# Kernel tuning notes

Hardware: AMD Instinct MI355X
Metric: run time of the kernel (lower is better)

## Reference

```python
import jax, jax.numpy as jnp
import numpy as np
import math
from jax.scipy.special import gammaln

D = 256
TOKEN_WEIGHT_TEMP = 0.5
BESSEL_TERMS = 50


def log_bessel_i(v, x, terms=BESSEL_TERMS):
    # log I_v(x) via truncated series, logsumexp-stabilized (same math as
    # torch max-subtract + exp-sum-log).
    x = jnp.clip(x, 1e-6)
    k = jnp.arange(terms, dtype=x.dtype)
    log_coef = (2.0 * k + v) * jnp.log(x[..., None] / 2.0) - (gammaln(k + 1.0) + gammaln(k + v + 1.0))
    return jax.nn.logsumexp(log_coef, axis=-1)


def vmf_A(kappa, d):
    kappa = jnp.clip(kappa, 1e-6)
    nu = 0.5 * d - 1.0
    A = jnp.exp(jnp.clip(log_bessel_i(nu + 1.0, kappa) - log_bessel_i(nu, kappa), -60.0, 0.0))
    return jnp.clip(A, 1e-8, 1.0 - 1e-6)


def vmf_logpartition(kappa, d):
    kappa = jnp.clip(kappa, 1e-6)
    nu = 0.5 * d - 1.0
    return nu * jnp.log(kappa) - 0.5 * d * math.log(2.0 * math.pi) - log_bessel_i(nu, kappa)


def vmf_entropy(kappa, d):
    kappa = jnp.clip(kappa, 1e-6)
    return -vmf_logpartition(kappa, d) - kappa * vmf_A(kappa, d)


def vmf_kl(kappa_p, mu_dot, kappa_q, d):
    kappa_p = jnp.clip(kappa_p, 1e-6)
    kappa_q = jnp.clip(kappa_q, 1e-6)
    logC_p = vmf_logpartition(kappa_p, d)
    logC_q = vmf_logpartition(kappa_q, d)
    A_p = vmf_A(kappa_p, d)
    return logC_p - logC_q + A_p * (kappa_p - kappa_q * mu_dot)


def setup_inputs() -> dict:
    key = jax.random.key(0)
    k1, k2, k3, k4 = jax.random.split(key, 4)
    B, Tq, N, Tt = 128, 32, 128, 32
    q = jax.random.normal(k1, (B, Tq, D), dtype=jnp.float32)
    q = q / jnp.linalg.norm(q, axis=-1, keepdims=True)
    t = jax.random.normal(k2, (N, Tt, D), dtype=jnp.float32)
    t = t / jnp.linalg.norm(t, axis=-1, keepdims=True)
    kq = jax.random.uniform(k3, (B, Tq), dtype=jnp.float32) * 50.0 + 1.0
    kt = jax.random.uniform(k4, (N, Tt), dtype=jnp.float32) * 50.0 + 1.0
    temp = jnp.asarray(0.07, dtype=jnp.float32)
    return {"query_tokens": q, "kappa_q_tokens": kq, "target_tokens": t, "kappa_t_tokens": kt, "temp": temp}


def reference(query_tokens, kappa_q_tokens, target_tokens, kappa_t_tokens, temp):
    bs = query_tokens.shape[0]
    labels = jnp.arange(bs)
    # sim: [B, N, T_t, T_q]
    sim_q2t = jnp.einsum('bqd,ntd->bntq', query_tokens, target_tokens)
    kappa_q_tokens = jnp.clip(kappa_q_tokens, 1e-6)
    kappa_t_tokens = jnp.clip(kappa_t_tokens, 1e-6)
    kq = kappa_q_tokens[:, None, None, :]   # [B,1,1,T_q]
    kt = kappa_t_tokens[None, :, :, None]   # [1,N,T_t,1]
    kl_q_t = vmf_kl(kq, sim_q2t, kt, D)
    kl_t_q = vmf_kl(kt, sim_q2t, kq, D)
    skl_qt = 0.5 * (kl_q_t + kl_t_q)
    score_q2t = -skl_qt                      # [B,N,T_t,T_q]
    max_score_i2t = score_q2t.max(axis=2)    # [B,N,T_q]
    entropy_q = vmf_entropy(kappa_q_tokens, D)  # [B,T_q]
    token_weights = jax.nn.softmax(-jax.lax.stop_gradient(entropy_q) / TOKEN_WEIGHT_TEMP, axis=-1)
    score_global = (max_score_i2t * token_weights[:, None, :]).sum(axis=-1)  # [B,N]
    logits_global = score_global / jnp.clip(temp, 1e-6)
    log_probs = jax.nn.log_softmax(logits_global, axis=-1)
    loss_each = -log_probs[jnp.arange(bs), labels]
    loss_itc = loss_each.mean()
    return (loss_itc, logits_global, score_global, entropy_q)
```

## Files before the change

kernel.cpp:

```cpp
#include <hip/hip_runtime.h>
#include <math.h>

typedef _Float16 half8  __attribute__((ext_vector_type(8)));
typedef _Float16 half4v __attribute__((ext_vector_type(4)));
typedef float    floatx4 __attribute__((ext_vector_type(4)));

#define DDIM 256

#define GLOAD_LDS16(g, l) \
    __builtin_amdgcn_global_load_lds((const __attribute__((address_space(1))) void*)(g), \
                                     (__attribute__((address_space(3))) void*)(l), 16, 0, 0)

__global__ void prep(const float* __restrict__ q, const float* __restrict__ t,
                     _Float16* __restrict__ Qh, _Float16* __restrict__ Th,
                     const float* __restrict__ kq, const float* __restrict__ kt,
                     float* __restrict__ Apq, float* __restrict__ kqc, float* __restrict__ uq,
                     float* __restrict__ wq,
                     float* __restrict__ At,  float* __restrict__ ktc, float* __restrict__ vt,
                     float* __restrict__ ent_out, float* __restrict__ loss) {
    int b = blockIdx.x;
    if (b < 2048) {
        const float* src = (b < 1024) ? q : t;
        _Float16*    dst = (b < 1024) ? Qh : Th;
        int i = ((b & 1023) * 1024) + threadIdx.x * 4;
        float4 v = *(const float4*)(src + i);
        half4v h;
        h[0] = (_Float16)v.x; h[1] = (_Float16)v.y; h[2] = (_Float16)v.z; h[3] = (_Float16)v.w;
        *(half4v*)(dst + i) = h;
        return;
    }

    __shared__ float slg_s[50];
    __shared__ float l128_s[50];
    int tid = threadIdx.x;

    if (b == 2048 && tid == 0) loss[0] = 0.f;

    if (tid < 64) {
        int lane = tid;
        float a = 0.f;
        if (lane >= 1 && lane < 50) a = logf((float)lane) + logf((float)(lane + 127));
        #pragma unroll
        for (int off = 1; off < 64; off <<= 1) {
            float tmp = __shfl_up(a, off, 64);
            if (lane >= off) a += tmp;
        }
        if (lane < 50) {
            slg_s[lane]  = 491.5534482233f + a;
            l128_s[lane] = logf((float)(lane + 128));
        }
    }
    __syncthreads();

    int tok  = (b - 2048) * 256 + tid;
    bool isQ = tok < 4096;
    float kap  = fmaxf(isQ ? kq[tok] : kt[tok - 4096], 1e-6f);
    float lkap = logf(kap);
    float lx   = lkap - 0.6931471805599453f;

    float m0 = -INFINITY, m1 = -INFINITY;
    #pragma unroll 10
    for (int k = 0; k < 50; ++k) {
        float c0 = fmaf((float)(2 * k + 127), lx, -slg_s[k]);
        float c1 = c0 + lx - l128_s[k];
        m0 = fmaxf(m0, c0);
        m1 = fmaxf(m1, c1);
    }
    float s0 = 0.f, s1 = 0.f;
    #pragma unroll 10
    for (int k = 0; k < 50; ++k) {
        float c0 = fmaf((float)(2 * k + 127), lx, -slg_s[k]);
        float c1 = c0 + lx - l128_s[k];
        s0 += expf(c0 - m0);
        s1 += expf(c1 - m1);
    }
    float logI0 = m0 + logf(s0);
    float logI1 = m1 + logf(s1);

    float A = expf(fminf(fmaxf(logI1 - logI0, -60.f), 0.f));
    A = fminf(fmaxf(A, 1e-8f), 1.f - 1e-6f);
    float logC = 127.f * lkap - 235.2482644983962f - logI0;
    float ent  = -logC - kap * A;

    if (isQ) {
        float x = -2.0f * ent;
        float m = x;
        #pragma unroll
        for (int off = 1; off < 32; off <<= 1) m = fmaxf(m, __shfl_xor(m, off, 64));
        float p = expf(x - m);
        float s = p;
        #pragma unroll
        for (int off = 1; off < 32; off <<= 1) s += __shfl_xor(s, off, 64);
        Apq[tok] = A; kqc[tok] = kap; uq[tok] = -0.5f * A * kap;
        wq[tok]  = p / s;
        ent_out[tok] = ent;
    } else {
        int tt = tok - 4096;
        At[tt] = A; ktc[tt] = kap; vt[tt] = -0.5f * A * kap;
    }
}

__global__ void __launch_bounds__(512, 2)
gemm_score(const _Float16* __restrict__ Qh, const _Float16* __restrict__ Th,
           const float* __restrict__ Apq, const float* __restrict__ kqc,
           const float* __restrict__ uq,  const float* __restrict__ wq,
           const float* __restrict__ At,  const float* __restrict__ ktc,
           const float* __restrict__ vt,  float* __restrict__ score_out) {
    __shared__ _Float16 Qs[2][256 * 64];
    __shared__ _Float16 Ts[2][256 * 64];
    int tid = threadIdx.x;
    int lane = tid & 63, wave = tid >> 6;
    int wr = wave >> 2, wc = wave & 3;
    int bx = blockIdx.x, by = blockIdx.y;

    floatx4 acc[8][4];
    #pragma unroll
    for (int i = 0; i < 8; ++i)
        #pragma unroll
        for (int j = 0; j < 4; ++j)
            acc[i][j] = (floatx4){0.f, 0.f, 0.f, 0.f};

    int l15 = lane & 15, lq = lane >> 4;
    int swz = l15 & 7;

    int rs = tid >> 3;
    int cl = tid & 7;
    int cg = cl ^ (rs & 7);
    const _Float16* gq = Qh + (size_t)(by * 256 + rs) * DDIM + cg * 8;
    const _Float16* gt = Th + (size_t)(bx * 256 + rs) * DDIM + cg * 8;
    int lbase = wave * 1024;

    #pragma unroll
    for (int it = 0; it < 4; ++it) {
        GLOAD_LDS16(gq + it * 64 * DDIM, (char*)Qs[0] + lbase + it * 8192);
        GLOAD_LDS16(gt + it * 64 * DDIM, (char*)Ts[0] + lbase + it * 8192);
    }

    #pragma unroll
    for (int kk = 0; kk < 4; ++kk) {
        int p = kk & 1;
        __syncthreads();
        if (kk < 3) {
            #pragma unroll
            for (int it = 0; it < 4; ++it) {
                GLOAD_LDS16(gq + it * 64 * DDIM + (kk + 1) * 64,
                            (char*)Qs[p ^ 1] + lbase + it * 8192);
                GLOAD_LDS16(gt + it * 64 * DDIM + (kk + 1) * 64,
                            (char*)Ts[p ^ 1] + lbase + it * 8192);
            }
        }
        #pragma unroll
        for (int ks = 0; ks < 2; ++ks) {
            half8 a[8], b[4];
            int chunk = (ks * 4 + lq) ^ swz;
            #pragma unroll
            for (int i = 0; i < 8; ++i)
                a[i] = *(const half8*)(Qs[p] + (wr * 128 + i * 16 + l15) * 64 + chunk * 8);
            #pragma unroll
            for (int j = 0; j < 4; ++j)
                b[j] = *(const half8*)(Ts[p] + (wc * 64 + j * 16 + l15) * 64 + chunk * 8);
            #pragma unroll
            for (int i = 0; i < 8; ++i)
                #pragma unroll
                for (int j = 0; j < 4; ++j)
                    acc[i][j] = __builtin_amdgcn_mfma_f32_16x16x32_f16(a[i], b[j], acc[i][j], 0, 0, 0);
        }
    }

    int colbase = bx * 256 + wc * 64 + l15;
    int rowbase = by * 256 + wr * 128 + lq * 4;
    #pragma unroll
    for (int bi = 0; bi < 4; ++bi) {
        #pragma unroll
        for (int bj = 0; bj < 2; ++bj) {
            float part = 0.f;
            #pragma unroll
            for (int ii = 0; ii < 2; ++ii) {
                int i  = bi * 2 + ii;
                int rg = rowbase + i * 16;
                float mx[4] = {-INFINITY, -INFINITY, -INFINITY, -INFINITY};
                #pragma unroll
                for (int jj = 0; jj < 2; ++jj) {
                    int j   = bj * 2 + jj;
                    int cg2 = colbase + j * 16;
                    float at_ = At[cg2], kt_ = ktc[cg2], v_ = vt[cg2];
                    floatx4 sim = acc[i][j];
                    #pragma unroll
                    for (int rr = 0; rr < 4; ++rr) {
                        float sc = uq[rg + rr] + v_ +
                                   0.5f * (Apq[rg + rr] * kt_ + at_ * kqc[rg + rr]) * sim[rr];
                        mx[rr] = fmaxf(mx[rr], sc);
                    }
                }
                #pragma unroll
                for (int msk = 1; msk <= 8; msk <<= 1)
                    #pragma unroll
                    for (int rr = 0; rr < 4; ++rr)
                        mx[rr] = fmaxf(mx[rr], __shfl_xor(mx[rr], msk, 64));
                if (l15 == 0) {
                    #pragma unroll
                    for (int rr = 0; rr < 4; ++rr)
                        part += wq[rg + rr] * mx[rr];
                }
            }
            part += __shfl_xor(part, 16, 64);
            part += __shfl_xor(part, 32, 64);
            if (lane == 0) {
                int b = by * 8 + wr * 4 + bi;
                int n = bx * 8 + wc * 2 + bj;
                score_out[b * 128 + n] = part;
            }
        }
    }
}

__global__ void softmax_loss(const float* __restrict__ score, const float* __restrict__ temp_p,
                             float* __restrict__ logits, float* __restrict__ loss) {
    int tid = threadIdx.x, lane = tid & 63, w = tid >> 6;
    int r = blockIdx.x * 8 + w;
    float temp = fmaxf(temp_p[0], 1e-6f);
    float inv = 1.0f / temp;

    float2 v = ((const float2*)(score + r * 128))[lane];
    v.x *= inv; v.y *= inv;
    float m = fmaxf(v.x, v.y);
    #pragma unroll
    for (int off = 1; off < 64; off <<= 1) m = fmaxf(m, __shfl_xor(m, off, 64));
    float e = expf(v.x - m) + expf(v.y - m);
    #pragma unroll
    for (int off = 1; off < 64; off <<= 1) e += __shfl_xor(e, off, 64);
    float lse = m + logf(e);

    ((float2*)(logits + r * 128))[lane] = v;

    if (lane == 0) {
        float le = lse - score[r * 129] * inv;
        atomicAdd(loss, le * (1.0f / 128.0f));
    }
}

extern "C" void kernel_launch(void* const* d_in, const int* in_sizes, int n_in,
                              void* d_out, int out_size, void* d_ws, size_t ws_size,
                              hipStream_t stream) {
    const float* q    = (const float*)d_in[0];
    const float* kq   = (const float*)d_in[1];
    const float* t    = (const float*)d_in[2];
    const float* kt   = (const float*)d_in[3];
    const float* temp = (const float*)d_in[4];

    float* out    = (float*)d_out;
    float* loss   = out;
    float* logits = out + 1;
    float* score  = out + 1 + 16384;
    float* ent    = out + 1 + 32768;

    char* ws = (char*)d_ws;
    _Float16* Qh = (_Float16*)(ws);
    _Float16* Th = (_Float16*)(ws + (1 << 21));
    float* stats = (float*)(ws + (1 << 22));
    float *Apq = stats,          *kqc = stats + 4096, *uq = stats + 8192,
          *wq  = stats + 12288,  *At  = stats + 16384, *ktc = stats + 20480,
          *vt  = stats + 24576;

    prep<<<2080, 256, 0, stream>>>(q, t, Qh, Th, kq, kt,
                                   Apq, kqc, uq, wq, At, ktc, vt, ent, loss);
    dim3 g(16, 16);
    gemm_score<<<g, 512, 0, stream>>>(Qh, Th, Apq, kqc, uq, wq, At, ktc, vt, score);
    softmax_loss<<<16, 512, 0, stream>>>(score, temp, logits, loss);
}
```

Measured before the change: 99.60 us.

## Fuse softmax/loss into GEMM via last-block counter and remap block tiles

Removes the separate softmax_loss launch by having the last GEMM block, detected with an atomic counter and threadfences, compute the log-softmax logits and the mean loss over all 128 rows. The 2D grid becomes a 1D grid with a remapped tile order that groups blocks for better L2 reuse of Q/T tiles. This saves one kernel launch but serializes the final softmax onto a single block after the GEMM tail.

```diff
diff --git a/kernel.cpp b/kernel.cpp
--- a/kernel.cpp
+++ b/kernel.cpp
@@ -17,7 +17,7 @@
                      float* __restrict__ Apq, float* __restrict__ kqc, float* __restrict__ uq,
                      float* __restrict__ wq,
                      float* __restrict__ At,  float* __restrict__ ktc, float* __restrict__ vt,
-                     float* __restrict__ ent_out, float* __restrict__ loss) {
+                     float* __restrict__ ent_out, int* __restrict__ counter) {
     int b = blockIdx.x;
     if (b < 2048) {
         const float* src = (b < 1024) ? q : t;
@@ -34,7 +34,7 @@
     __shared__ float l128_s[50];
     int tid = threadIdx.x;
 
-    if (b == 2048 && tid == 0) loss[0] = 0.f;
+    if (b == 2048 && tid == 0) counter[0] = 0;
 
     if (tid < 64) {
         int lane = tid;
@@ -105,13 +105,19 @@
            const float* __restrict__ Apq, const float* __restrict__ kqc,
            const float* __restrict__ uq,  const float* __restrict__ wq,
            const float* __restrict__ At,  const float* __restrict__ ktc,
-           const float* __restrict__ vt,  float* __restrict__ score_out) {
+           const float* __restrict__ vt,  float* __restrict__ score_out,
+           const float* __restrict__ temp_p, float* __restrict__ logits,
+           float* __restrict__ loss, int* __restrict__ counter) {
     __shared__ _Float16 Qs[2][256 * 64];
     __shared__ _Float16 Ts[2][256 * 64];
     int tid = threadIdx.x;
     int lane = tid & 63, wave = tid >> 6;
     int wr = wave >> 2, wc = wave & 3;
-    int bx = blockIdx.x, by = blockIdx.y;
+
+    int bid = blockIdx.x;
+    int g = bid & 7, ii_ = bid >> 3;
+    int bx = (g & 3) * 4 + (ii_ & 3);
+    int by = (g >> 2) * 8 + (ii_ >> 2);
 
     floatx4 acc[8][4];
     #pragma unroll
@@ -175,8 +181,8 @@
         for (int bj = 0; bj < 2; ++bj) {
             float part = 0.f;
             #pragma unroll
-            for (int ii = 0; ii < 2; ++ii) {
-                int i  = bi * 2 + ii;
+            for (int ii2 = 0; ii2 < 2; ++ii2) {
+                int i  = bi * 2 + ii2;
                 int rg = rowbase + i * 16;
                 float mx[4] = {-INFINITY, -INFINITY, -INFINITY, -INFINITY};
                 #pragma unroll
@@ -212,30 +218,42 @@
             }
         }
     }
-}
-
-__global__ void softmax_loss(const float* __restrict__ score, const float* __restrict__ temp_p,
-                             float* __restrict__ logits, float* __restrict__ loss) {
-    int tid = threadIdx.x, lane = tid & 63, w = tid >> 6;
-    int r = blockIdx.x * 8 + w;
+
+    __shared__ int lastFlag;
+    __shared__ float lpart[8];
+    __threadfence();
+    if (tid == 0) {
+        int old = atomicAdd(counter, 1);
+        lastFlag = (old == 255);
+    }
+    __syncthreads();
+    if (!lastFlag) return;
+    __threadfence();
+
     float temp = fmaxf(temp_p[0], 1e-6f);
     float inv = 1.0f / temp;
-
-    float2 v = ((const float2*)(score + r * 128))[lane];
-    v.x *= inv; v.y *= inv;
-    float m = fmaxf(v.x, v.y);
-    #pragma unroll
-    for (int off = 1; off < 64; off <<= 1) m = fmaxf(m, __shfl_xor(m, off, 64));
-    float e = expf(v.x - m) + expf(v.y - m);
-    #pragma unroll
-    for (int off = 1; off < 64; off <<= 1) e += __shfl_xor(e, off, 64);
-    float lse = m + logf(e);
-
-    ((float2*)(logits + r * 128))[lane] = v;
-
-    if (lane == 0) {
-        float le = lse - score[r * 129] * inv;
-        atomicAdd(loss, le * (1.0f / 128.0f));
+    float lsum = 0.f;
+    for (int rr = 0; rr < 16; ++rr) {
+        int r = wave * 16 + rr;
+        float2 v = ((const float2*)(score_out + r * 128))[lane];
+        v.x *= inv; v.y *= inv;
+        float m = fmaxf(v.x, v.y);
+        #pragma unroll
+        for (int off = 1; off < 64; off <<= 1) m = fmaxf(m, __shfl_xor(m, off, 64));
+        float e = expf(v.x - m) + expf(v.y - m);
+        #pragma unroll
+        for (int off = 1; off < 64; off <<= 1) e += __shfl_xor(e, off, 64);
+        float lse = m + logf(e);
+        ((float2*)(logits + r * 128))[lane] = v;
+        if (lane == 0) lsum += lse - score_out[r * 129] * inv;
+    }
+    if (lane == 0) lpart[wave] = lsum;
+    __syncthreads();
+    if (tid == 0) {
+        float s = 0.f;
+        #pragma unroll
+        for (int i = 0; i < 8; ++i) s += lpart[i];
+        loss[0] = s * (1.0f / 128.0f);
     }
 }
 
@@ -261,10 +279,10 @@
     float *Apq = stats,          *kqc = stats + 4096, *uq = stats + 8192,
           *wq  = stats + 12288,  *At  = stats + 16384, *ktc = stats + 20480,
           *vt  = stats + 24576;
+    int* counter = (int*)(stats + 28672);
 
     prep<<<2080, 256, 0, stream>>>(q, t, Qh, Th, kq, kt,
-                                   Apq, kqc, uq, wq, At, ktc, vt, ent, loss);
-    dim3 g(16, 16);
-    gemm_score<<<g, 512, 0, stream>>>(Qh, Th, Apq, kqc, uq, wq, At, ktc, vt, score);
-    softmax_loss<<<16, 512, 0, stream>>>(score, temp, logits, loss);
+                                   Apq, kqc, uq, wq, At, ktc, vt, ent, counter);
+    gemm_score<<<256, 512, 0, stream>>>(Qh, Th, Apq, kqc, uq, wq, At, ktc, vt, score,
+                                        temp, logits, loss, counter);
 }
```

New measurement: 143.1 us. 43.7% more time.
